# Optimization experiments

Hardware: AMD Instinct MI355X
Metric: run time of the kernel (lower is better)

The kernel has to match this reference:

```python
import jax, jax.numpy as jnp
import numpy as np


def setup_inputs() -> dict:
    key = jax.random.key(0)
    k1, k2 = jax.random.split(key)
    # probabilities strictly inside (0,1) so log(x) and log(1-x) are finite
    input = jax.random.uniform(k1, (16384, 4096), dtype=jnp.float32) * 0.98 + 0.01
    target = jax.random.randint(k2, (16384, 4096), 0, 2, dtype=jnp.int32)
    return {"input": input, "target": target}


def reference(input, target):
    x = input.reshape(-1)
    t = target.reshape(-1)
    n = x.shape[0]                      # static Python int
    tf = t.astype(x.dtype)
    s = tf.sum()                        # number of positives
    length = jnp.asarray(n + 1, x.dtype)
    wp = length / (s + 1)               # positive-class weight
    wn = length / (length - s)          # negative-class weight
    # fused masked elementwise + reduction (targets not in {0,1} contribute 0)
    pos = jnp.where(t == 1, -jnp.log(x), jnp.zeros((), x.dtype)).sum()
    neg = jnp.where(t == 0, -jnp.log1p(-x), jnp.zeros((), x.dtype)).sum()
    loss = ((wp + 1) * pos + (wn + 1) * neg) / n
    return loss
```

## Files before the change

kernel.cpp:

```cpp
#include <hip/hip_runtime.h>

#define BLOCK 256
#define GRID 2048
#define UNROLL 4

__global__ __launch_bounds__(BLOCK) void wbce_reduce_kernel(
    const float* __restrict__ x, const int* __restrict__ t,
    long long n, double* __restrict__ ws) {
    const long long n4 = n >> 2;
    const long long idx = (long long)blockIdx.x * BLOCK + threadIdx.x;
    const long long stride = (long long)GRID * BLOCK;

    float tot = 0.0f, pos = 0.0f;
    int cnt = 0;

    const float4* __restrict__ x4 = (const float4*)x;
    const int4*   __restrict__ t4 = (const int4*)t;

#define PROC(XC, TC)                                        \
    {                                                       \
        float xi = (XC); int ti = (TC);                     \
        float a = ti ? xi : (1.0f - xi);                    \
        float v = -__logf(a);                               \
        tot += v;                                           \
        pos += ti ? v : 0.0f;                               \
        cnt += ti ? 1 : 0;                                  \
    }

    const long long chunk = stride * UNROLL;
    const long long n4_main = n4 - (n4 % chunk);

    for (long long base = idx; base < n4_main; base += chunk) {
        float4 xv[UNROLL];
        int4   tv[UNROLL];
#pragma unroll
        for (int j = 0; j < UNROLL; ++j)
            xv[j] = x4[base + (long long)j * stride];
#pragma unroll
        for (int j = 0; j < UNROLL; ++j)
            tv[j] = t4[base + (long long)j * stride];
#pragma unroll
        for (int j = 0; j < UNROLL; ++j) {
            PROC(xv[j].x, tv[j].x)
            PROC(xv[j].y, tv[j].y)
            PROC(xv[j].z, tv[j].z)
            PROC(xv[j].w, tv[j].w)
        }
    }

    for (long long i = n4_main + idx; i < n4; i += stride) {
        float4 xv = x4[i];
        int4   tv = t4[i];
        PROC(xv.x, tv.x)
        PROC(xv.y, tv.y)
        PROC(xv.z, tv.z)
        PROC(xv.w, tv.w)
    }

    if (idx == 0) {
        for (long long i = n4 << 2; i < n; ++i) {
            float xi = x[i]; int ti = t[i];
            float a = ti ? xi : (1.0f - xi);
            float v = -__logf(a);
            tot += v;
            pos += ti ? v : 0.0f;
            cnt += ti ? 1 : 0;
        }
    }
#undef PROC

    float neg = tot - pos;

    for (int o = 32; o > 0; o >>= 1) {
        pos += __shfl_down(pos, o);
        neg += __shfl_down(neg, o);
        cnt += __shfl_down(cnt, o);
    }

    __shared__ float s_pos[BLOCK / 64];
    __shared__ float s_neg[BLOCK / 64];
    __shared__ int   s_cnt[BLOCK / 64];
    const int lane = threadIdx.x & 63;
    const int wave = threadIdx.x >> 6;
    if (lane == 0) {
        s_pos[wave] = pos;
        s_neg[wave] = neg;
        s_cnt[wave] = cnt;
    }
    __syncthreads();

    if (threadIdx.x == 0) {
        double bpos = 0.0, bneg = 0.0;
        long long bcnt = 0;
        for (int w = 0; w < BLOCK / 64; ++w) {
            bpos += (double)s_pos[w];
            bneg += (double)s_neg[w];
            bcnt += s_cnt[w];
        }
        atomicAdd(&ws[0], (double)bcnt);
        atomicAdd(&ws[1], bpos);
        atomicAdd(&ws[2], bneg);
    }
}

__global__ void wbce_finalize_kernel(const double* __restrict__ ws,
                                     float* __restrict__ out, double n) {
    double s   = ws[0];
    double pos = ws[1];
    double neg = ws[2];
    double len = n + 1.0;
    double wp  = len / (s + 1.0);
    double wn  = len / (len - s);
    double loss = ((wp + 1.0) * pos + (wn + 1.0) * neg) / n;
    out[0] = (float)loss;
}

extern "C" void kernel_launch(void* const* d_in, const int* in_sizes, int n_in,
                              void* d_out, int out_size, void* d_ws, size_t ws_size,
                              hipStream_t stream) {
    const float* x = (const float*)d_in[0];
    const int*   t = (const int*)d_in[1];
    float* out = (float*)d_out;
    double* ws = (double*)d_ws;
    const long long n = (long long)in_sizes[0];

    hipMemsetAsync(ws, 0, 3 * sizeof(double), stream);
    wbce_reduce_kernel<<<GRID, BLOCK, 0, stream>>>(x, t, n, ws);
    wbce_finalize_kernel<<<1, 1, 0, stream>>>(ws, out, (double)n);
}
```

Before: 140.9 us.

## Use contiguous per-block chunks, 32-bit indexing, log2 with deferred ln2 scaling

Each block now walks its own contiguous slab of the arrays with an 8-way unroll, instead of the old grid-strided interleaving. Indexing switches to 32-bit arithmetic to cut address computation. The per-element natural log is replaced by log2, with the ln2 factor applied once in the finalize kernel, which saves a multiply per element. The mask count is simplified to add the target directly. Together these aim to raise memory-level parallelism and trim ALU work in a bandwidth-bound reduction, at the cost of more registers and an int-overflow assumption on the element count.

```diff
diff --git a/kernel.cpp b/kernel.cpp
--- a/kernel.cpp
+++ b/kernel.cpp
@@ -2,14 +2,17 @@
 
 #define BLOCK 256
 #define GRID 2048
-#define UNROLL 4
+#define UNROLL 8
 
 __global__ __launch_bounds__(BLOCK) void wbce_reduce_kernel(
     const float* __restrict__ x, const int* __restrict__ t,
     long long n, double* __restrict__ ws) {
-    const long long n4 = n >> 2;
-    const long long idx = (long long)blockIdx.x * BLOCK + threadIdx.x;
-    const long long stride = (long long)GRID * BLOCK;
+    const int n4 = (int)(n >> 2);
+    const int tid = threadIdx.x;
+
+    const int per_iter = BLOCK * UNROLL;
+    const int iters_total = n4 / (GRID * per_iter);
+    const int main_count = GRID * per_iter * iters_total;
 
     float tot = 0.0f, pos = 0.0f;
     int cnt = 0;
@@ -21,24 +24,22 @@
     {                                                       \
         float xi = (XC); int ti = (TC);                     \
         float a = ti ? xi : (1.0f - xi);                    \
-        float v = -__logf(a);                               \
+        float v = -__log2f(a);                              \
         tot += v;                                           \
         pos += ti ? v : 0.0f;                               \
-        cnt += ti ? 1 : 0;                                  \
+        cnt += ti;                                          \
     }
 
-    const long long chunk = stride * UNROLL;
-    const long long n4_main = n4 - (n4 % chunk);
-
-    for (long long base = idx; base < n4_main; base += chunk) {
+    int base = blockIdx.x * per_iter * iters_total + tid;
+    for (int it = 0; it < iters_total; ++it, base += per_iter) {
         float4 xv[UNROLL];
         int4   tv[UNROLL];
 #pragma unroll
         for (int j = 0; j < UNROLL; ++j)
-            xv[j] = x4[base + (long long)j * stride];
+            xv[j] = x4[base + j * BLOCK];
 #pragma unroll
         for (int j = 0; j < UNROLL; ++j)
-            tv[j] = t4[base + (long long)j * stride];
+            tv[j] = t4[base + j * BLOCK];
 #pragma unroll
         for (int j = 0; j < UNROLL; ++j) {
             PROC(xv[j].x, tv[j].x)
@@ -48,7 +49,7 @@
         }
     }
 
-    for (long long i = n4_main + idx; i < n4; i += stride) {
+    for (int i = main_count + blockIdx.x * BLOCK + tid; i < n4; i += GRID * BLOCK) {
         float4 xv = x4[i];
         int4   tv = t4[i];
         PROC(xv.x, tv.x)
@@ -57,14 +58,14 @@
         PROC(xv.w, tv.w)
     }
 
-    if (idx == 0) {
-        for (long long i = n4 << 2; i < n; ++i) {
+    if (blockIdx.x == 0 && tid == 0) {
+        for (long long i = (long long)n4 << 2; i < n; ++i) {
             float xi = x[i]; int ti = t[i];
             float a = ti ? xi : (1.0f - xi);
-            float v = -__logf(a);
+            float v = -__log2f(a);
             tot += v;
             pos += ti ? v : 0.0f;
-            cnt += ti ? 1 : 0;
+            cnt += ti;
         }
     }
 #undef PROC
@@ -80,8 +81,8 @@
     __shared__ float s_pos[BLOCK / 64];
     __shared__ float s_neg[BLOCK / 64];
     __shared__ int   s_cnt[BLOCK / 64];
-    const int lane = threadIdx.x & 63;
-    const int wave = threadIdx.x >> 6;
+    const int lane = tid & 63;
+    const int wave = tid >> 6;
     if (lane == 0) {
         s_pos[wave] = pos;
         s_neg[wave] = neg;
@@ -89,7 +90,7 @@
     }
     __syncthreads();
 
-    if (threadIdx.x == 0) {
+    if (tid == 0) {
         double bpos = 0.0, bneg = 0.0;
         long long bcnt = 0;
         for (int w = 0; w < BLOCK / 64; ++w) {
@@ -105,9 +106,10 @@
 
 __global__ void wbce_finalize_kernel(const double* __restrict__ ws,
                                      float* __restrict__ out, double n) {
+    const double LN2 = 0.6931471805599453;
     double s   = ws[0];
-    double pos = ws[1];
-    double neg = ws[2];
+    double pos = ws[1] * LN2;
+    double neg = ws[2] * LN2;
     double len = n + 1.0;
     double wp  = len / (s + 1.0);
     double wn  = len / (len - s);
```

New measurement: 142.0 us. No clear change (+0.7%).
